# Kernel optimization log

Hardware: AMD Instinct MI355X
Metric: run time of the kernel (lower is better)

## Reference

```python
import jax, jax.numpy as jnp
import numpy as np

DIM, HEADS, DHEAD, CTX_DIM, DFF = 1280, 20, 64, 768, 5120
EPS = 1e-5
SCALE = DHEAD ** -0.5


def layer_norm(x, g, b):
    mu = jnp.mean(x, axis=-1, keepdims=True)
    var = jnp.mean(jnp.square(x - mu), axis=-1, keepdims=True)
    return (x - mu) * jax.lax.rsqrt(var + EPS) * g + b


def cross_attention(x, ctx, wq, wk, wv, wo, bo):
    B, N, _ = x.shape
    M = ctx.shape[1]
    q = jnp.einsum('bne,ef->bnf', x, wq).reshape(B, N, HEADS, DHEAD).transpose(0, 2, 1, 3)
    k = jnp.einsum('bme,ef->bmf', ctx, wk).reshape(B, M, HEADS, DHEAD).transpose(0, 2, 1, 3)
    v = jnp.einsum('bme,ef->bmf', ctx, wv).reshape(B, M, HEADS, DHEAD).transpose(0, 2, 1, 3)
    scores = jnp.einsum('bhnd,bhmd->bhnm', q, k) * SCALE
    attn = jax.nn.softmax(scores, axis=-1)
    out = jnp.einsum('bhnm,bhmd->bhnd', attn, v)
    out = out.transpose(0, 2, 1, 3).reshape(B, N, HEADS * DHEAD)
    return jnp.einsum('bnf,fe->bne', out, wo) + bo


def geglu_ff(x, w1, b1, w2, b2):
    h = jnp.einsum('bne,ef->bnf', x, w1) + b1  # [B,N,2*DFF]
    a, gate = h[..., :DFF], h[..., DFF:]
    h = a * jax.nn.gelu(gate)
    return jnp.einsum('bnf,fe->bne', h, w2) + b2


def block_forward(x, context,
                  g1, be1, wq1, wk1, wv1, wo1, bo1,
                  g2, be2, wq2, wk2, wv2, wo2, bo2,
                  g3, be3, w_ff1, b_ff1, w_ff2, b_ff2):
    x = cross_attention(layer_norm(x, g1, be1), layer_norm(x, g1, be1), wq1, wk1, wv1, wo1, bo1) + x
    x = cross_attention(layer_norm(x, g2, be2), context, wq2, wk2, wv2, wo2, bo2) + x
    return geglu_ff(layer_norm(x, g3, be3), w_ff1, b_ff1, w_ff2, b_ff2) + x


def setup_inputs() -> dict:
    key = jax.random.key(0)
    ks = jax.random.split(key, 20)
    s = 0.02
    inner = HEADS * DHEAD
    return {
        'x': jax.random.normal(ks[0], (4, 1024, DIM), jnp.float32),
        'context': jax.random.normal(ks[1], (4, 77, CTX_DIM), jnp.float32),
        'g1': jnp.ones((DIM,), jnp.float32), 'be1': jnp.zeros((DIM,), jnp.float32),
        'wq1': jax.random.normal(ks[2], (DIM, inner), jnp.float32) * s,
        'wk1': jax.random.normal(ks[3], (DIM, inner), jnp.float32) * s,
        'wv1': jax.random.normal(ks[4], (DIM, inner), jnp.float32) * s,
        'wo1': jax.random.normal(ks[5], (inner, DIM), jnp.float32) * s,
        'bo1': jnp.zeros((DIM,), jnp.float32),
        'g2': jnp.ones((DIM,), jnp.float32), 'be2': jnp.zeros((DIM,), jnp.float32),
        'wq2': jax.random.normal(ks[6], (DIM, inner), jnp.float32) * s,
        'wk2': jax.random.normal(ks[7], (CTX_DIM, inner), jnp.float32) * s,
        'wv2': jax.random.normal(ks[8], (CTX_DIM, inner), jnp.float32) * s,
        'wo2': jax.random.normal(ks[9], (inner, DIM), jnp.float32) * s,
        'bo2': jnp.zeros((DIM,), jnp.float32),
        'g3': jnp.ones((DIM,), jnp.float32), 'be3': jnp.zeros((DIM,), jnp.float32),
        'w_ff1': jax.random.normal(ks[10], (DIM, 2 * DFF), jnp.float32) * s,
        'b_ff1': jnp.zeros((2 * DFF,), jnp.float32),
        'w_ff2': jax.random.normal(ks[11], (DFF, DIM), jnp.float32) * s,
        'b_ff2': jnp.zeros((DIM,), jnp.float32),
    }


def reference(x, context,
              g1, be1, wq1, wk1, wv1, wo1, bo1,
              g2, be2, wq2, wk2, wv2, wo2, bo2,
              g3, be3, w_ff1, b_ff1, w_ff2, b_ff2):
    return block_forward(x, context,
                         g1, be1, wq1, wk1, wv1, wo1, bo1,
                         g2, be2, wq2, wk2, wv2, wo2, bo2,
                         g3, be3, w_ff1, b_ff1, w_ff2, b_ff2)
```

## Files before the change

kernel.cpp:

```cpp
#include <hip/hip_runtime.h>

typedef unsigned short u16;
typedef __bf16 bf16x8 __attribute__((ext_vector_type(8)));
typedef float f32x4 __attribute__((ext_vector_type(4)));

static __device__ __forceinline__ float bf2f(u16 u) {
    union { unsigned int i; float f; } v; v.i = ((unsigned int)u) << 16; return v.f;
}
static __device__ __forceinline__ u16 f2bf(float f) {
    union { float f; unsigned int i; } v; v.f = f;
    unsigned int b = v.i;
    b += 0x7fffu + ((b >> 16) & 1u);
    return (u16)(b >> 16);
}
static __device__ __forceinline__ u16 ldbf(const void* p, size_t i, int isf32) {
    return isf32 ? f2bf(((const float*)p)[i]) : ((const u16*)p)[i];
}
static __device__ __forceinline__ float ldf(const void* p, size_t i, int isf32) {
    return isf32 ? ((const float*)p)[i] : bf2f(((const u16*)p)[i]);
}
static __device__ __forceinline__ void glds16(const u16* g, u16* l) {
    __builtin_amdgcn_global_load_lds(
        (const __attribute__((address_space(1))) unsigned int*)g,
        (__attribute__((address_space(3))) unsigned int*)l,
        16, 0, 0);
}

__global__ __launch_bounds__(256) void k_detect(const u16* __restrict__ xu, int* __restrict__ flag) {
    u16 v = xu[threadIdx.x * 2];
    int e = (v >> 7) & 0xFF;
    int sane = (e >= 87 && e <= 133) ? 1 : 0;
    int total = __syncthreads_count(sane);
    if (threadIdx.x == 0) flag[0] = (total < 192) ? 1 : 0;
}

__global__ __launch_bounds__(256) void k_b2f(const void* __restrict__ in, float* __restrict__ out, int n,
                                             const int* __restrict__ flagp) {
    int isf32 = *flagp;
    int i = blockIdx.x * 256 + threadIdx.x;
    if (i < n) out[i] = ldf(in, i, isf32);
}

__global__ __launch_bounds__(256) void k_cvt(const void* __restrict__ in, u16* __restrict__ out, int n,
                                             const int* __restrict__ flagp) {
    int isf32 = *flagp;
    int i = blockIdx.x * 256 + threadIdx.x;
    if (i < n) out[i] = ldbf(in, i, isf32);
}

__global__ __launch_bounds__(256) void k_transpose(const void* __restrict__ W, u16* __restrict__ Wt,
                                                   int K, int N, const int* __restrict__ flagp) {
    int isf32 = *flagp;
    __shared__ u16 T[32][33];
    int k0 = blockIdx.x * 32, n0 = blockIdx.y * 32;
    int tid = threadIdx.x;
    int c = tid & 31, rr = tid >> 5;
    #pragma unroll
    for (int j = 0; j < 4; ++j) {
        int k = rr + j * 8;
        T[k][c] = ldbf(W, (size_t)(k0 + k) * N + n0 + c, isf32);
    }
    __syncthreads();
    #pragma unroll
    for (int j = 0; j < 4; ++j) {
        int n = rr + j * 8;
        Wt[(size_t)(n0 + n) * K + k0 + c] = T[c][n];
    }
}

__global__ __launch_bounds__(256) void k_layernorm(const float* __restrict__ X, const void* __restrict__ G,
                                                   const void* __restrict__ Bb, u16* __restrict__ Y, int D,
                                                   const int* __restrict__ flagp) {
    int isf32 = *flagp;
    int row = blockIdx.x;
    const float* xr = X + (size_t)row * D;
    float s = 0.f, s2 = 0.f;
    for (int i = threadIdx.x; i < D; i += 256) { float v = xr[i]; s += v; s2 += v * v; }
    #pragma unroll
    for (int off = 32; off; off >>= 1) { s += __shfl_down(s, off); s2 += __shfl_down(s2, off); }
    __shared__ float rs[4], rs2[4];
    __shared__ float stat[2];
    int w = threadIdx.x >> 6;
    if ((threadIdx.x & 63) == 0) { rs[w] = s; rs2[w] = s2; }
    __syncthreads();
    if (threadIdx.x == 0) {
        float ts = rs[0] + rs[1] + rs[2] + rs[3];
        float ts2 = rs2[0] + rs2[1] + rs2[2] + rs2[3];
        float mu = ts / D;
        float var = ts2 / D - mu * mu;
        stat[0] = mu; stat[1] = rsqrtf(var + 1e-5f);
    }
    __syncthreads();
    float mu = stat[0], rstd = stat[1];
    u16* yr = Y + (size_t)row * D;
    for (int i = threadIdx.x; i < D; i += 256) {
        yr[i] = f2bf((xr[i] - mu) * rstd * ldf(G, i, isf32) + ldf(Bb, i, isf32));
    }
}

template <int EPI>
__global__ __launch_bounds__(256) void k_gemm_t(const u16* __restrict__ A, const u16* __restrict__ Bt,
                                                void* __restrict__ Cout, float* __restrict__ Rf,
                                                const void* __restrict__ bias,
                                                int M, int N, int K, const int* __restrict__ flagp) {
    int isf32 = *flagp;
    __shared__ __align__(16) u16 As[4096];
    __shared__ __align__(16) u16 Bs[4096];
    int tid = threadIdx.x;
    int row0 = blockIdx.x * 128, col0 = blockIdx.y * 128;
    int wave = tid >> 6, lane = tid & 63;
    int wm = (wave >> 1) * 64, wn = (wave & 1) * 64;
    int quad = lane >> 4, r = lane & 15;
    int c0 = wave * 64 + lane, c1 = 256 + c0;
    int ar0 = c0 >> 2, aq0 = (c0 & 3) ^ ((ar0 >> 1) & 3);
    int ar1 = c1 >> 2, aq1 = (c1 & 3) ^ ((ar1 >> 1) & 3);
    const u16* Ag0 = A + (size_t)min(row0 + ar0, M - 1) * K + aq0 * 8;
    const u16* Ag1 = A + (size_t)min(row0 + ar1, M - 1) * K + aq1 * 8;
    const u16* Bg0 = Bt + (size_t)(col0 + ar0) * K + aq0 * 8;
    const u16* Bg1 = Bt + (size_t)(col0 + ar1) * K + aq1 * 8;
    u16* lA0 = As + wave * 512;
    u16* lA1 = As + 2048 + wave * 512;
    u16* lB0 = Bs + wave * 512;
    u16* lB1 = Bs + 2048 + wave * 512;
    f32x4 acc[4][4] = {};
    for (int k0 = 0; k0 < K; k0 += 32) {
        __syncthreads();
        glds16(Ag0 + k0, lA0);
        glds16(Ag1 + k0, lA1);
        glds16(Bg0 + k0, lB0);
        glds16(Bg1 + k0, lB1);
        __syncthreads();
        bf16x8 af[4], bfv[4];
        #pragma unroll
        for (int i = 0; i < 4; ++i) {
            int row = wm + i * 16 + r;
            af[i] = *(const bf16x8*)(As + (row * 4 + (quad ^ ((row >> 1) & 3))) * 8);
        }
        #pragma unroll
        for (int g = 0; g < 4; ++g) {
            int row = wn + g * 16 + r;
            bfv[g] = *(const bf16x8*)(Bs + (row * 4 + (quad ^ ((row >> 1) & 3))) * 8);
        }
        #pragma unroll
        for (int i = 0; i < 4; ++i)
            #pragma unroll
            for (int g = 0; g < 4; ++g)
                acc[i][g] = __builtin_amdgcn_mfma_f32_16x16x32_bf16(af[i], bfv[g], acc[i][g], 0, 0, 0);
    }
    #pragma unroll
    for (int i = 0; i < 4; ++i) {
        int grow = row0 + wm + i * 16 + quad * 4;
        if (grow >= M) continue;
        #pragma unroll
        for (int g = 0; g < 4; ++g) {
            int gcol = col0 + wn + g * 16 + r;
            float bv = (EPI == 2) ? ldf(bias, gcol, isf32) : 0.f;
            #pragma unroll
            for (int t = 0; t < 4; ++t) {
                float v = acc[i][g][t];
                size_t off = (size_t)(grow + t) * N + gcol;
                if (EPI == 0) ((u16*)Cout)[off] = f2bf(v);
                else Rf[off] += v + bv;
            }
        }
    }
}

__global__ __launch_bounds__(256) void k_geglu_t(const u16* __restrict__ A, const u16* __restrict__ Bt,
                                                 const void* __restrict__ bias, u16* __restrict__ Out,
                                                 int M, int K, const int* __restrict__ flagp) {
    const int Nout = 5120;
    int isf32 = *flagp;
    __shared__ __align__(16) u16 As[4096];
    __shared__ __align__(16) u16 Bs[4096];
    int tid = threadIdx.x;
    int row0 = blockIdx.x * 128, col0 = blockIdx.y * 64;
    int wave = tid >> 6, lane = tid & 63;
    int quad = lane >> 4, r = lane & 15;
    int c0 = wave * 64 + lane, c1 = 256 + c0;
    int ar0 = c0 >> 2, aq0 = (c0 & 3) ^ ((ar0 >> 1) & 3);
    int ar1 = c1 >> 2, aq1 = (c1 & 3) ^ ((ar1 >> 1) & 3);
    const u16* Ag0 = A + (size_t)min(row0 + ar0, M - 1) * K + aq0 * 8;
    const u16* Ag1 = A + (size_t)min(row0 + ar1, M - 1) * K + aq1 * 8;
    const u16* Bg0 = Bt + (size_t)((ar0 >> 6) * Nout + col0 + (ar0 & 63)) * K + aq0 * 8;
    const u16* Bg1 = Bt + (size_t)((ar1 >> 6) * Nout + col0 + (ar1 & 63)) * K + aq1 * 8;
    u16* lA0 = As + wave * 512;
    u16* lA1 = As + 2048 + wave * 512;
    u16* lB0 = Bs + wave * 512;
    u16* lB1 = Bs + 2048 + wave * 512;
    f32x4 acc[2][2][4] = {};
    for (int k0 = 0; k0 < K; k0 += 32) {
        __syncthreads();
        glds16(Ag0 + k0, lA0);
        glds16(Ag1 + k0, lA1);
        glds16(Bg0 + k0, lB0);
        glds16(Bg1 + k0, lB1);
        __syncthreads();
        bf16x8 af[2], bv[2][4];
        #pragma unroll
        for (int i = 0; i < 2; ++i) {
            int row = wave * 32 + i * 16 + r;
            af[i] = *(const bf16x8*)(As + (row * 4 + (quad ^ ((row >> 1) & 3))) * 8);
        }
        #pragma unroll
        for (int p = 0; p < 2; ++p)
            #pragma unroll
            for (int g = 0; g < 4; ++g) {
                int row = p * 64 + g * 16 + r;
                bv[p][g] = *(const bf16x8*)(Bs + (row * 4 + (quad ^ ((row >> 1) & 3))) * 8);
            }
        #pragma unroll
        for (int p = 0; p < 2; ++p)
            #pragma unroll
            for (int i = 0; i < 2; ++i)
                #pragma unroll
                for (int g = 0; g < 4; ++g)
                    acc[p][i][g] = __builtin_amdgcn_mfma_f32_16x16x32_bf16(af[i], bv[p][g], acc[p][i][g], 0, 0, 0);
    }
    #pragma unroll
    for (int i = 0; i < 2; ++i) {
        int grow = row0 + wave * 32 + i * 16 + quad * 4;
        #pragma unroll
        for (int g = 0; g < 4; ++g) {
            int gcol = col0 + g * 16 + r;
            float bva = ldf(bias, gcol, isf32);
            float bvu = ldf(bias, Nout + gcol, isf32);
            #pragma unroll
            for (int t = 0; t < 4; ++t) {
                float a = acc[0][i][g][t] + bva;
                float u = acc[1][i][g][t] + bvu;
                float z2 = 1.5957691216f * (u + 0.044715f * u * u * u);
                float gl = u * __builtin_amdgcn_rcpf(1.f + __expf(-z2));
                Out[(size_t)(grow + t) * Nout + gcol] = f2bf(a * gl);
            }
        }
    }
}

template <int EPI, bool AEXT>
__global__ __launch_bounds__(256) void k_gemm(const void* __restrict__ A, const void* __restrict__ B,
                                              void* __restrict__ Cout, float* __restrict__ Rf,
                                              const void* __restrict__ bias,
                                              int M, int N, int K, const int* __restrict__ flagp) {
    int isf32 = *flagp;
    __shared__ u16 As[64][40];
    __shared__ u16 Bs[64][40];
    int tid = threadIdx.x;
    int row0 = blockIdx.x * 64, col0 = blockIdx.y * 64;
    int wave = tid >> 6, lane = tid & 63;
    int wm = (wave >> 1) * 32, wn = (wave & 1) * 32;
    int quad = lane >> 4, r = lane & 15;
    int arow = tid >> 2, akk = (tid & 3) * 8;
    int bnl = tid & 63, bkk = (tid >> 6) * 8;
    int garow = row0 + arow;
    f32x4 acc[2][2] = {};
    for (int k0 = 0; k0 < K; k0 += 32) {
        uint4 aval = {0u, 0u, 0u, 0u};
        if (garow < M) {
            if (AEXT && isf32) {
                const float* Af = (const float*)A;
                u16 t[8];
                #pragma unroll
                for (int j = 0; j < 8; ++j) t[j] = f2bf(Af[(size_t)garow * K + k0 + akk + j]);
                aval = *(uint4*)t;
            } else {
                aval = *(const uint4*)((const u16*)A + (size_t)garow * K + k0 + akk);
            }
        }
        u16 btmp[8];
        #pragma unroll
        for (int j = 0; j < 8; ++j) btmp[j] = ldbf(B, (size_t)(k0 + bkk + j) * N + col0 + bnl, isf32);
        __syncthreads();
        *(uint4*)(&As[arow][akk]) = aval;
        *(uint4*)(&Bs[bnl][bkk]) = *(uint4*)btmp;
        __syncthreads();
        bf16x8 a0 = *(const bf16x8*)(&As[wm + r][quad * 8]);
        bf16x8 a1 = *(const bf16x8*)(&As[wm + 16 + r][quad * 8]);
        bf16x8 b0 = *(const bf16x8*)(&Bs[wn + r][quad * 8]);
        bf16x8 b1 = *(const bf16x8*)(&Bs[wn + 16 + r][quad * 8]);
        acc[0][0] = __builtin_amdgcn_mfma_f32_16x16x32_bf16(a0, b0, acc[0][0], 0, 0, 0);
        acc[0][1] = __builtin_amdgcn_mfma_f32_16x16x32_bf16(a0, b1, acc[0][1], 0, 0, 0);
        acc[1][0] = __builtin_amdgcn_mfma_f32_16x16x32_bf16(a1, b0, acc[1][0], 0, 0, 0);
        acc[1][1] = __builtin_amdgcn_mfma_f32_16x16x32_bf16(a1, b1, acc[1][1], 0, 0, 0);
    }
    #pragma unroll
    for (int i = 0; i < 2; ++i)
        #pragma unroll
        for (int jn = 0; jn < 2; ++jn)
            #pragma unroll
            for (int t = 0; t < 4; ++t) {
                int grow = row0 + wm + i * 16 + quad * 4 + t;
                int gcol = col0 + wn + jn * 16 + r;
                if (grow >= M) continue;
                float v = acc[i][jn][t];
                size_t off = (size_t)grow * N + gcol;
                if (EPI == 0) {
                    ((u16*)Cout)[off] = f2bf(v);
                } else if (EPI == 2) {
                    Rf[off] += v + ldf(bias, gcol, isf32);
                } else {
                    ((float*)Cout)[off] = v + ldf(bias, gcol, isf32) + Rf[off];
                }
            }
}

__global__ __launch_bounds__(256) void k_gemm_geglu(const u16* __restrict__ A, const void* __restrict__ B,
                                                    const void* __restrict__ bias, u16* __restrict__ Out,
                                                    int M, int Nout, int K, int ldb,
                                                    const int* __restrict__ flagp) {
    int isf32 = *flagp;
    __shared__ u16 As[64][40];
    __shared__ u16 Bs[64][40];
    int tid = threadIdx.x;
    int row0 = blockIdx.x * 64, col0 = blockIdx.y * 64;
    int wave = tid >> 6, lane = tid & 63;
    int wm = (wave >> 1) * 32, wn = (wave & 1) * 32;
    int quad = lane >> 4, r = lane & 15;
    int arow = tid >> 2, akk = (tid & 3) * 8;
    int bnl = tid & 63, bkk = (tid >> 6) * 8;
    int garow = row0 + arow;
    f32x4 acc[2][2][2] = {};
    for (int p = 0; p < 2; ++p) {
        for (int k0 = 0; k0 < K; k0 += 32) {
            uint4 aval = {0u, 0u, 0u, 0u};
            if (garow < M) aval = *(const uint4*)(A + (size_t)garow * K + k0 + akk);
            u16 btmp[8];
            #pragma unroll
            for (int j = 0; j < 8; ++j)
                btmp[j] = ldbf(B, (size_t)(k0 + bkk + j) * ldb + p * Nout + col0 + bnl, isf32);
            __syncthreads();
            *(uint4*)(&As[arow][akk]) = aval;
            *(uint4*)(&Bs[bnl][bkk]) = *(uint4*)btmp;
            __syncthreads();
            bf16x8 a0 = *(const bf16x8*)(&As[wm + r][quad * 8]);
            bf16x8 a1 = *(const bf16x8*)(&As[wm + 16 + r][quad * 8]);
            bf16x8 b0 = *(const bf16x8*)(&Bs[wn + r][quad * 8]);
            bf16x8 b1 = *(const bf16x8*)(&Bs[wn + 16 + r][quad * 8]);
            acc[p][0][0] = __builtin_amdgcn_mfma_f32_16x16x32_bf16(a0, b0, acc[p][0][0], 0, 0, 0);
            acc[p][0][1] = __builtin_amdgcn_mfma_f32_16x16x32_bf16(a0, b1, acc[p][0][1], 0, 0, 0);
            acc[p][1][0] = __builtin_amdgcn_mfma_f32_16x16x32_bf16(a1, b0, acc[p][1][0], 0, 0, 0);
            acc[p][1][1] = __builtin_amdgcn_mfma_f32_16x16x32_bf16(a1, b1, acc[p][1][1], 0, 0, 0);
        }
    }
    #pragma unroll
    for (int i = 0; i < 2; ++i)
        #pragma unroll
        for (int jn = 0; jn < 2; ++jn)
            #pragma unroll
            for (int t = 0; t < 4; ++t) {
                int grow = row0 + wm + i * 16 + quad * 4 + t;
                int gcol = col0 + wn + jn * 16 + r;
                if (grow >= M) continue;
                float a = acc[0][i][jn][t] + ldf(bias, gcol, isf32);
                float u = acc[1][i][jn][t] + ldf(bias, Nout + gcol, isf32);
                float th = tanhf(0.7978845608f * (u + 0.044715f * u * u * u));
                float gl = 0.5f * u * (1.f + th);
                Out[(size_t)grow * Nout + gcol] = f2bf(a * gl);
            }
}

__global__ __launch_bounds__(256) void k_attn_flash(const u16* __restrict__ Q, const u16* __restrict__ K,
                                                    const u16* __restrict__ V, u16* __restrict__ O,
                                                    int N, int Mkv, int H, int ldq, int ldkv, int ldo) {
    __shared__ u16 Sp[4][16][40];
    __shared__ u16 VT[64][40];
    int nt = N / 64;
    int qt = blockIdx.x % nt;
    int bh = blockIdx.x / nt;
    int h = bh % H, b = bh / H;
    int tid = threadIdx.x, wave = tid >> 6, lane = tid & 63;
    int quad = lane >> 4, r = lane & 15;
    int q0 = qt * 64 + wave * 16;

    const u16* qbase = Q + ((size_t)(b * N + q0 + r)) * ldq + h * 64;
    bf16x8 aq0 = *(const bf16x8*)(qbase + quad * 8);
    bf16x8 aq1 = *(const bf16x8*)(qbase + 32 + quad * 8);

    f32x4 accO[4] = {};
    float m_i[4] = {-1e30f, -1e30f, -1e30f, -1e30f};
    float l_i[4] = {0.f, 0.f, 0.f, 0.f};

    int vkv = tid & 31, vdg = tid >> 5;

    for (int kv0 = 0; kv0 < Mkv; kv0 += 32) {
        int kr0 = min(kv0 + r, Mkv - 1);
        int kr1 = min(kv0 + 16 + r, Mkv - 1);
        const u16* kb0 = K + ((size_t)(b * Mkv + kr0)) * ldkv + h * 64;
        const u16* kb1 = K + ((size_t)(b * Mkv + kr1)) * ldkv + h * 64;
        bf16x8 bk00 = *(const bf16x8*)(kb0 + quad * 8);
        bf16x8 bk01 = *(const bf16x8*)(kb0 + 32 + quad * 8);
        bf16x8 bk10 = *(const bf16x8*)(kb1 + quad * 8);
        bf16x8 bk11 = *(const bf16x8*)(kb1 + 32 + quad * 8);
        int vrow = min(kv0 + vkv, Mkv - 1);
        uint4 vv = *(const uint4*)(V + ((size_t)(b * Mkv + vrow)) * ldkv + h * 64 + vdg * 8);

        __syncthreads();
        VT[vdg * 8 + 0][vkv] = (u16)(vv.x);
        VT[vdg * 8 + 1][vkv] = (u16)(vv.x >> 16);
        VT[vdg * 8 + 2][vkv] = (u16)(vv.y);
        VT[vdg * 8 + 3][vkv] = (u16)(vv.y >> 16);
        VT[vdg * 8 + 4][vkv] = (u16)(vv.z);
        VT[vdg * 8 + 5][vkv] = (u16)(vv.z >> 16);
        VT[vdg * 8 + 6][vkv] = (u16)(vv.w);
        VT[vdg * 8 + 7][vkv] = (u16)(vv.w >> 16);
        __syncthreads();

        f32x4 s0 = {}, s1 = {};
        s0 = __builtin_amdgcn_mfma_f32_16x16x32_bf16(aq0, bk00, s0, 0, 0, 0);
        s0 = __builtin_amdgcn_mfma_f32_16x16x32_bf16(aq1, bk01, s0, 0, 0, 0);
        s1 = __builtin_amdgcn_mfma_f32_16x16x32_bf16(aq0, bk10, s1, 0, 0, 0);
        s1 = __builtin_amdgcn_mfma_f32_16x16x32_bf16(aq1, bk11, s1, 0, 0, 0);
        bool mask0 = (kv0 + r) >= Mkv;
        bool mask1 = (kv0 + 16 + r) >= Mkv;

        #pragma unroll
        for (int t = 0; t < 4; ++t) {
            float a = mask0 ? -1e30f : s0[t] * 0.125f;
            float c = mask1 ? -1e30f : s1[t] * 0.125f;
            float mx = fmaxf(a, c);
            mx = fmaxf(mx, __shfl_xor(mx, 1));
            mx = fmaxf(mx, __shfl_xor(mx, 2));
            mx = fmaxf(mx, __shfl_xor(mx, 4));
            mx = fmaxf(mx, __shfl_xor(mx, 8));
            float mn = fmaxf(m_i[t], mx);
            float alpha = __expf(m_i[t] - mn);
            float p0 = __expf(a - mn);
            float p1 = __expf(c - mn);
            float ps = p0 + p1;
            ps += __shfl_xor(ps, 1);
            ps += __shfl_xor(ps, 2);
            ps += __shfl_xor(ps, 4);
            ps += __shfl_xor(ps, 8);
            l_i[t] = l_i[t] * alpha + ps;
            m_i[t] = mn;
            accO[0][t] *= alpha; accO[1][t] *= alpha; accO[2][t] *= alpha; accO[3][t] *= alpha;
            Sp[wave][quad * 4 + t][r] = f2bf(p0);
            Sp[wave][quad * 4 + t][16 + r] = f2bf(p1);
        }

        bf16x8 ap = *(const bf16x8*)(&Sp[wave][r][quad * 8]);
        #pragma unroll
        for (int g = 0; g < 4; ++g) {
            bf16x8 bvv = *(const bf16x8*)(&VT[g * 16 + r][quad * 8]);
            accO[g] = __builtin_amdgcn_mfma_f32_16x16x32_bf16(ap, bvv, accO[g], 0, 0, 0);
        }
    }

    u16* ob = O + ((size_t)(b * N + q0)) * ldo + h * 64;
    #pragma unroll
    for (int t = 0; t < 4; ++t) {
        float inv = 1.f / l_i[t];
        #pragma unroll
        for (int g = 0; g < 4; ++g)
            ob[(size_t)(quad * 4 + t) * ldo + g * 16 + r] = f2bf(accO[g][t] * inv);
    }
}

extern "C" void kernel_launch(void* const* d_in, const int* in_sizes, int n_in,
                              void* d_out, int out_size, void* d_ws, size_t ws_size,
                              hipStream_t stream) {
    const void* x    = d_in[0];
    const void* ctx  = d_in[1];
    const void* g1   = d_in[2];
    const void* be1  = d_in[3];
    const void* wq1  = d_in[4];
    const void* wk1  = d_in[5];
    const void* wv1  = d_in[6];
    const void* wo1  = d_in[7];
    const void* bo1  = d_in[8];
    const void* g2   = d_in[9];
    const void* be2  = d_in[10];
    const void* wq2  = d_in[11];
    const void* wk2  = d_in[12];
    const void* wv2  = d_in[13];
    const void* wo2  = d_in[14];
    const void* bo2  = d_in[15];
    const void* g3   = d_in[16];
    const void* be3  = d_in[17];
    const void* wff1 = d_in[18];
    const void* bff1 = d_in[19];
    const void* wff2 = d_in[20];
    const void* bff2 = d_in[21];

    const int BT = 4096, D = 1280;
    dim3 blk(256);
    char* ws = (char*)d_ws;

    const size_t NEED_FAST = 117393664;
    if (ws_size >= NEED_FAST) {
        int*   flag   = (int*)(ws);
        u16* lnout    = (u16*)(ws + 256);
        u16* qkv      = (u16*)(ws + 10486016);
        u16* attnout  = (u16*)(ws + 10486016 + 31457280);
        u16* gbuf     = (u16*)(ws + 10486016);
        u16* ctxb     = (u16*)(ws + 52429056);
        u16* kv2      = (u16*)(ws + 52902144);
        u16* wqkv1t   = (u16*)(ws + 54479104);
        u16* wo1t     = (u16*)(ws + 64309504);
        u16* wq2t     = (u16*)(ws + 67586304);
        u16* wkv2t    = (u16*)(ws + 70863104);
        u16* wo2t     = (u16*)(ws + 74795264);
        u16* wff1t    = (u16*)(ws + 78072064);
        u16* wff2t    = (u16*)(ws + 104286464);
        float* xres   = (float*)d_out;

        k_detect<<<dim3(1), blk, 0, stream>>>((const u16*)x, flag);
        k_b2f<<<dim3((BT * D + 255) / 256), blk, 0, stream>>>(x, xres, BT * D, flag);
        k_transpose<<<dim3(40, 40), blk, 0, stream>>>(wq1, wqkv1t, 1280, 1280, flag);
        k_transpose<<<dim3(40, 40), blk, 0, stream>>>(wk1, wqkv1t + 1280 * 1280, 1280, 1280, flag);
        k_transpose<<<dim3(40, 40), blk, 0, stream>>>(wv1, wqkv1t + 2 * 1280 * 1280, 1280, 1280, flag);
        k_transpose<<<dim3(40, 40), blk, 0, stream>>>(wo1, wo1t, 1280, 1280, flag);
        k_transpose<<<dim3(40, 40), blk, 0, stream>>>(wq2, wq2t, 1280, 1280, flag);
        k_transpose<<<dim3(24, 40), blk, 0, stream>>>(wk2, wkv2t, 768, 1280, flag);
        k_transpose<<<dim3(24, 40), blk, 0, stream>>>(wv2, wkv2t + 1280 * 768, 768, 1280, flag);
        k_transpose<<<dim3(40, 40), blk, 0, stream>>>(wo2, wo2t, 1280, 1280, flag);
        k_transpose<<<dim3(40, 320), blk, 0, stream>>>(wff1, wff1t, 1280, 10240, flag);
        k_transpose<<<dim3(160, 40), blk, 0, stream>>>(wff2, wff2t, 5120, 1280, flag);
        k_cvt<<<dim3((308 * 768 + 255) / 256), blk, 0, stream>>>(ctx, ctxb, 308 * 768, flag);
        k_layernorm<<<dim3(BT), blk, 0, stream>>>(xres, g1, be1, lnout, D, flag);
        k_gemm_t<0><<<dim3(32, 30), blk, 0, stream>>>(lnout, wqkv1t, qkv, nullptr, nullptr, BT, 3840, D, flag);
        k_attn_flash<<<dim3(16 * 80), blk, 0, stream>>>(qkv, qkv + 1280, qkv + 2560, attnout,
                                                        1024, 1024, 20, 3840, 3840, 1280);
        k_gemm_t<2><<<dim3(32, 10), blk, 0, stream>>>(attnout, wo1t, nullptr, xres, bo1, BT, D, D, flag);
        k_layernorm<<<dim3(BT), blk, 0, stream>>>(xres, g2, be2, lnout, D, flag);
        k_gemm_t<0><<<dim3(32, 10), blk, 0, stream>>>(lnout, wq2t, qkv, nullptr, nullptr, BT, D, D, flag);
        k_gemm_t<0><<<dim3(3, 20), blk, 0, stream>>>(ctxb, wkv2t, kv2, nullptr, nullptr, 308, 2560, 768, flag);
        k_attn_flash<<<dim3(16 * 80), blk, 0, stream>>>(qkv, kv2, kv2 + 1280, attnout,
                                                        1024, 77, 20, 1280, 2560, 1280);
        k_gemm_t<2><<<dim3(32, 10), blk, 0, stream>>>(attnout, wo2t, nullptr, xres, bo2, BT, D, D, flag);
        k_layernorm<<<dim3(BT), blk, 0, stream>>>(xres, g3, be3, lnout, D, flag);
        k_geglu_t<<<dim3(32, 80), blk, 0, stream>>>(lnout, wff1t, bff1, gbuf, BT, D, flag);
        k_gemm_t<2><<<dim3(32, 10), blk, 0, stream>>>(gbuf, wff2t, nullptr, xres, bff2, BT, D, 5120, flag);
    } else {
        int*   flag    = (int*)(ws);
        float* xres    = (float*)(ws + 256);
        u16* lnout     = (u16*)(ws + 20971776);
        u16* q         = (u16*)(ws + 31457536);
        u16* kbuf      = (u16*)(ws + 41943296);
        u16* vbuf      = (u16*)(ws + 52429056);
        u16* attnout   = (u16*)(ws + 62914816);
        u16* k2        = (u16*)(ws + 73400576);
        u16* v2        = (u16*)(ws + 74189056);
        u16* gbuf      = (u16*)(ws + 31457536);

        dim3 g_gemm(64, 20);
        dim3 g_kv(5, 20);
        dim3 g_attn(16 * 80);

        k_detect<<<dim3(1), blk, 0, stream>>>((const u16*)x, flag);
        k_b2f<<<dim3((BT * D + 255) / 256), blk, 0, stream>>>(x, xres, BT * D, flag);
        k_layernorm<<<dim3(BT), blk, 0, stream>>>(xres, g1, be1, lnout, D, flag);
        k_gemm<0, false><<<g_gemm, blk, 0, stream>>>(lnout, wq1, q, nullptr, nullptr, BT, D, D, flag);
        k_gemm<0, false><<<g_gemm, blk, 0, stream>>>(lnout, wk1, kbuf, nullptr, nullptr, BT, D, D, flag);
        k_gemm<0, false><<<g_gemm, blk, 0, stream>>>(lnout, wv1, vbuf, nullptr, nullptr, BT, D, D, flag);
        k_attn_flash<<<g_attn, blk, 0, stream>>>(q, kbuf, vbuf, attnout, 1024, 1024, 20, 1280, 1280, 1280);
        k_gemm<2, false><<<g_gemm, blk, 0, stream>>>(attnout, wo1, nullptr, xres, bo1, BT, D, D, flag);
        k_layernorm<<<dim3(BT), blk, 0, stream>>>(xres, g2, be2, lnout, D, flag);
        k_gemm<0, false><<<g_gemm, blk, 0, stream>>>(lnout, wq2, q, nullptr, nullptr, BT, D, D, flag);
        k_gemm<0, true><<<g_kv, blk, 0, stream>>>(ctx, wk2, k2, nullptr, nullptr, 308, D, 768, flag);
        k_gemm<0, true><<<g_kv, blk, 0, stream>>>(ctx, wv2, v2, nullptr, nullptr, 308, D, 768, flag);
        k_attn_flash<<<g_attn, blk, 0, stream>>>(q, k2, v2, attnout, 1024, 77, 20, 1280, 1280, 1280);
        k_gemm<2, false><<<g_gemm, blk, 0, stream>>>(attnout, wo2, nullptr, xres, bo2, BT, D, D, flag);
        k_layernorm<<<dim3(BT), blk, 0, stream>>>(xres, g3, be3, lnout, D, flag);
        k_gemm_geglu<<<dim3(64, 80), blk, 0, stream>>>(lnout, wff1, bff1, gbuf, BT, 5120, D, 10240, flag);
        k_gemm<3, false><<<g_gemm, blk, 0, stream>>>(gbuf, wff2, d_out, xres, bff2, BT, D, 5120, flag);
    }
}
```

Before: 918.3 us.

## Add 256x256-tile 8-wave GEMM with fused GEGLU for QKV and FF1

Adds a new GEMM kernel that uses 512-thread blocks, 256x256 output tiles, a 128 KB double-buffered LDS pipeline fed by direct global-to-LDS loads, and loads for the next K tile interleaved between the MFMA sub-phases. A second epilogue variant fuses bias and a GEGLU gate computed with a sigmoid-based GELU approximation, and interleaves the a and gate columns so each wave holds both halves. The kernel replaces the QKV projection GEMM and the FF1 GEGLU GEMM, aiming for more data reuse per tile and better overlap of loads with compute. The larger tiles produce fewer blocks (240 for QKV) across the GPU's compute units, and the heavy LDS use limits how many blocks each CU can hold.

```diff
diff --git a/kernel.cpp b/kernel.cpp
--- a/kernel.cpp
+++ b/kernel.cpp
@@ -95,6 +95,150 @@
     u16* yr = Y + (size_t)row * D;
     for (int i = threadIdx.x; i < D; i += 256) {
         yr[i] = f2bf((xr[i] - mu) * rstd * ldf(G, i, isf32) + ldf(Bb, i, isf32));
+    }
+}
+
+template <int EPI>
+__global__ __launch_bounds__(512, 2) void k_gemm8(const u16* __restrict__ A, const u16* __restrict__ Bt,
+                                                  void* __restrict__ Cout, const void* __restrict__ bias,
+                                                  int M, int N, int K, const int* __restrict__ flagp) {
+    __shared__ __align__(16) u16 sm[65536];
+    const int tid = threadIdx.x;
+    const int w = tid >> 6;
+    const int lane = tid & 63;
+    const int quad = lane >> 4, r = lane & 15;
+    const int wm = w >> 2, wn = w & 3;
+    const int row0 = blockIdx.x * 256, col0 = blockIdx.y * 256;
+    const int NT = K >> 6;
+
+    const u16* aP[2][2];
+    const u16* bP[2][2];
+    #pragma unroll
+    for (int j = 0; j < 2; ++j) {
+        int c = tid + w * 64 + j * 64;
+        int rj = c >> 3;
+        int qe = (c & 7) ^ (rj & 7);
+        #pragma unroll
+        for (int h = 0; h < 2; ++h) {
+            int gr = h * 128 + rj;
+            aP[h][j] = A + (size_t)(row0 + gr) * K + qe * 8;
+            int n = col0 + gr;
+            int m = (EPI == 1) ? (((n >> 4) & 1) * 5120 + (n >> 5) * 16 + (n & 15)) : n;
+            bP[h][j] = Bt + (size_t)m * K + qe * 8;
+        }
+    }
+    auto stageA = [&](int h, int t) {
+        u16* base = sm + (t & 1) * 32768 + h * 8192 + w * 1024;
+        glds16(aP[h][0] + t * 64, base);
+        glds16(aP[h][1] + t * 64, base + 512);
+    };
+    auto stageB = [&](int h, int t) {
+        u16* base = sm + (t & 1) * 32768 + 16384 + h * 8192 + w * 1024;
+        glds16(bP[h][0] + t * 64, base);
+        glds16(bP[h][1] + t * 64, base + 512);
+    };
+
+    stageA(0, 0); stageB(0, 0); stageA(1, 0); stageB(1, 0);
+    if (NT > 1) {
+        stageA(0, 1); stageB(0, 1);
+        asm volatile("s_waitcnt vmcnt(4)" ::: "memory");
+    } else {
+        asm volatile("s_waitcnt vmcnt(0)" ::: "memory");
+    }
+    __builtin_amdgcn_s_barrier();
+
+    f32x4 acc[2][2][4][2] = {};
+    const int xq = r & 7;
+    for (int t = 0; t < NT; ++t) {
+        const int Ab = (t & 1) * 32768;
+        const int Bb = Ab + 16384;
+        #pragma unroll
+        for (int qp = 0; qp < 4; ++qp) {
+            const int qm = qp >> 1, qn = qp & 1;
+            bf16x8 af[4][2], bf[2][2];
+            #pragma unroll
+            for (int i = 0; i < 4; ++i) {
+                int ar = qm * 128 + wm * 64 + i * 16 + r;
+                #pragma unroll
+                for (int ks = 0; ks < 2; ++ks)
+                    af[i][ks] = *(const bf16x8*)(sm + Ab + ar * 64 + (((ks * 4 + quad) ^ xq) * 8));
+            }
+            #pragma unroll
+            for (int g = 0; g < 2; ++g) {
+                int br = qn * 128 + wn * 32 + g * 16 + r;
+                #pragma unroll
+                for (int ks = 0; ks < 2; ++ks)
+                    bf[g][ks] = *(const bf16x8*)(sm + Bb + br * 64 + (((ks * 4 + quad) ^ xq) * 8));
+            }
+            if (qp == 0)      { if (t + 1 < NT) stageA(1, t + 1); }
+            else if (qp == 1) { if (t + 1 < NT) stageB(1, t + 1); }
+            else if (qp == 2) { if (t + 2 < NT) stageA(0, t + 2); }
+            else              { if (t + 2 < NT) stageB(0, t + 2); }
+            __builtin_amdgcn_s_barrier();
+            asm volatile("s_waitcnt lgkmcnt(0)" ::: "memory");
+            __builtin_amdgcn_sched_barrier(0);
+            __builtin_amdgcn_s_setprio(1);
+            #pragma unroll
+            for (int ks = 0; ks < 2; ++ks)
+                #pragma unroll
+                for (int i = 0; i < 4; ++i)
+                    #pragma unroll
+                    for (int g = 0; g < 2; ++g)
+                        acc[qm][qn][i][g] = __builtin_amdgcn_mfma_f32_16x16x32_bf16(
+                            af[i][ks], bf[g][ks], acc[qm][qn][i][g], 0, 0, 0);
+            __builtin_amdgcn_s_setprio(0);
+            if (qp == 3) {
+                if (t + 2 < NT) asm volatile("s_waitcnt vmcnt(4)" ::: "memory");
+                else            asm volatile("s_waitcnt vmcnt(0)" ::: "memory");
+            }
+            __builtin_amdgcn_s_barrier();
+        }
+    }
+
+    if (EPI == 0) {
+        u16* C = (u16*)Cout;
+        #pragma unroll
+        for (int qm = 0; qm < 2; ++qm) {
+            #pragma unroll
+            for (int qn = 0; qn < 2; ++qn) {
+                #pragma unroll
+                for (int i = 0; i < 4; ++i) {
+                    int grow = row0 + qm * 128 + wm * 64 + i * 16 + quad * 4;
+                    #pragma unroll
+                    for (int g = 0; g < 2; ++g) {
+                        int gcol = col0 + qn * 128 + wn * 32 + g * 16 + r;
+                        #pragma unroll
+                        for (int t4 = 0; t4 < 4; ++t4)
+                            C[(size_t)(grow + t4) * N + gcol] = f2bf(acc[qm][qn][i][g][t4]);
+                    }
+                }
+            }
+        }
+    } else {
+        const int isf32 = *flagp;
+        u16* C = (u16*)Cout;
+        #pragma unroll
+        for (int qm = 0; qm < 2; ++qm) {
+            #pragma unroll
+            for (int qn = 0; qn < 2; ++qn) {
+                int ncb = col0 + qn * 128 + wn * 32;
+                int oc = (ncb >> 1) + r;
+                float bva = ldf(bias, oc, isf32);
+                float bvu = ldf(bias, 5120 + oc, isf32);
+                #pragma unroll
+                for (int i = 0; i < 4; ++i) {
+                    int grow = row0 + qm * 128 + wm * 64 + i * 16 + quad * 4;
+                    #pragma unroll
+                    for (int t4 = 0; t4 < 4; ++t4) {
+                        float a = acc[qm][qn][i][0][t4] + bva;
+                        float u = acc[qm][qn][i][1][t4] + bvu;
+                        float z2 = 1.5957691216f * (u + 0.044715f * u * u * u);
+                        float gl = u * __builtin_amdgcn_rcpf(1.f + __expf(-z2));
+                        C[(size_t)(grow + t4) * 5120 + oc] = f2bf(a * gl);
+                    }
+                }
+            }
+        }
     }
 }
 
@@ -518,7 +662,7 @@
         k_transpose<<<dim3(160, 40), blk, 0, stream>>>(wff2, wff2t, 5120, 1280, flag);
         k_cvt<<<dim3((308 * 768 + 255) / 256), blk, 0, stream>>>(ctx, ctxb, 308 * 768, flag);
         k_layernorm<<<dim3(BT), blk, 0, stream>>>(xres, g1, be1, lnout, D, flag);
-        k_gemm_t<0><<<dim3(32, 30), blk, 0, stream>>>(lnout, wqkv1t, qkv, nullptr, nullptr, BT, 3840, D, flag);
+        k_gemm8<0><<<dim3(16, 15), dim3(512), 0, stream>>>(lnout, wqkv1t, qkv, nullptr, BT, 3840, D, flag);
         k_attn_flash<<<dim3(16 * 80), blk, 0, stream>>>(qkv, qkv + 1280, qkv + 2560, attnout,
                                                         1024, 1024, 20, 3840, 3840, 1280);
         k_gemm_t<2><<<dim3(32, 10), blk, 0, stream>>>(attnout, wo1t, nullptr, xres, bo1, BT, D, D, flag);
@@ -529,7 +673,7 @@
                                                         1024, 77, 20, 1280, 2560, 1280);
         k_gemm_t<2><<<dim3(32, 10), blk, 0, stream>>>(attnout, wo2t, nullptr, xres, bo2, BT, D, D, flag);
         k_layernorm<<<dim3(BT), blk, 0, stream>>>(xres, g3, be3, lnout, D, flag);
-        k_geglu_t<<<dim3(32, 80), blk, 0, stream>>>(lnout, wff1t, bff1, gbuf, BT, D, flag);
+        k_gemm8<1><<<dim3(16, 40), dim3(512), 0, stream>>>(lnout, wff1t, gbuf, bff1, BT, 10240, D, flag);
         k_gemm_t<2><<<dim3(32, 10), blk, 0, stream>>>(gbuf, wff2t, nullptr, xres, bff2, BT, D, 5120, flag);
     } else {
         int*   flag    = (int*)(ws);
```

After: 875.9 us. 4.6% less time.
